# Kernel tuning notes

Hardware: AMD Instinct MI355X
Metric: run time of the kernel (lower is better)

The kernel has to match this reference:

```python
import jax, jax.numpy as jnp
import numpy as np

MAX_OBJECTS = 20
NODE_FEAT_DIM = 16
N_COLORS = 10
N_OPS = 8
HID = 64
RANK = 4
B = 32768


def _layer_norm(x, gamma, beta, eps=1e-5):
    mu = x.mean(-1, keepdims=True)
    var = ((x - mu) ** 2).mean(-1, keepdims=True)
    return (x - mu) / jnp.sqrt(var + eps) * gamma + beta


def setup_inputs() -> dict:
    key = jax.random.key(0)
    ks = jax.random.split(key, 32)
    lin = lambda k, i, o: jax.random.normal(k, (i, o), jnp.float32) * (1.0 / np.sqrt(i))
    d = {}
    d['nf'] = jax.random.normal(ks[0], (B, MAX_OBJECTS, NODE_FEAT_DIM), jnp.float32)
    d['nn_c'] = jax.random.randint(ks[1], (B,), 1, MAX_OBJECTS + 1)
    # ne + its LoRA adapter
    d['ne_W'] = lin(ks[2], NODE_FEAT_DIM, HID); d['ne_b'] = jnp.zeros((HID,), jnp.float32)
    d['ne_A'] = jax.random.normal(ks[3], (NODE_FEAT_DIM, RANK), jnp.float32) * 0.01
    d['ne_B'] = jax.random.normal(ks[4], (RANK, HID), jnp.float32) * 0.01
    # g1: Linear(2*hid,hid) [LoRA-wrapped] then Linear(hid,hid); relu applied after in lora path
    d['g1_W0'] = lin(ks[5], 2 * HID, HID); d['g1_b0'] = jnp.zeros((HID,), jnp.float32)
    d['g1_A'] = jax.random.normal(ks[6], (2 * HID, RANK), jnp.float32) * 0.01
    d['g1_B'] = jax.random.normal(ks[7], (RANK, HID), jnp.float32) * 0.01
    d['g1_W2'] = lin(ks[8], HID, HID); d['g1_b2'] = jnp.zeros((HID,), jnp.float32)
    d['g2_W0'] = lin(ks[9], 2 * HID, HID); d['g2_b0'] = jnp.zeros((HID,), jnp.float32)
    d['g2_A'] = jax.random.normal(ks[10], (2 * HID, RANK), jnp.float32) * 0.01
    d['g2_B'] = jax.random.normal(ks[11], (RANK, HID), jnp.float32) * 0.01
    d['g2_W2'] = lin(ks[12], HID, HID); d['g2_b2'] = jnp.zeros((HID,), jnp.float32)
    d['n1_g'] = jnp.ones((HID,), jnp.float32); d['n1_b'] = jnp.zeros((HID,), jnp.float32)
    d['n2_g'] = jnp.ones((HID,), jnp.float32); d['n2_b'] = jnp.zeros((HID,), jnp.float32)
    d['oh_W'] = lin(ks[13], HID, N_OPS); d['oh_b'] = jnp.zeros((N_OPS,), jnp.float32)
    d['c1_W'] = lin(ks[14], HID, N_COLORS); d['c1_b'] = jnp.zeros((N_COLORS,), jnp.float32)
    d['c2_W'] = lin(ks[15], HID, N_COLORS); d['c2_b'] = jnp.zeros((N_COLORS,), jnp.float32)
    d['pq_W'] = lin(ks[16], HID, HID); d['pq_b'] = jnp.zeros((HID,), jnp.float32)
    d['pk_W'] = lin(ks[17], HID, HID); d['pk_b'] = jnp.zeros((HID,), jnp.float32)
    return d


def reference(nf, nn_c, ne_W, ne_b, ne_A, ne_B,
              g1_W0, g1_b0, g1_A, g1_B, g1_W2, g1_b2,
              g2_W0, g2_b0, g2_A, g2_B, g2_W2, g2_b2,
              n1_g, n1_b, n2_g, n2_b,
              oh_W, oh_b, c1_W, c1_b, c2_W, c2_b, pq_W, pq_b, pk_W, pk_b):
    mask = jnp.arange(MAX_OBJECTS)[None, :] < nn_c[:, None]            # [B, N]
    mf = mask.astype(nf.dtype)[..., None]                              # [B, N, 1]
    denom = jnp.clip(mf.sum(1, keepdims=True), 1.0, None)              # [B, 1, 1]

    # node embedding with LoRA
    h = nf @ ne_W + ne_b + (nf @ ne_A) @ ne_B                          # [B, N, hid]

    def gnn_layer(h, W0, b0, A, Bm, W2, b2, lg, lb):
        msg = (h * mf).sum(1, keepdims=True) / denom                   # [B, 1, hid]
        cat = jnp.concatenate([h, jnp.broadcast_to(msg, h.shape)], -1) # [B, N, 2*hid]
        z = cat @ W0 + b0 + (cat @ A) @ Bm                             # LoRA linear
        h = h + jax.nn.relu(z @ W2 + b2)                               # relu AFTER second linear (lora path)
        return _layer_norm(h, lg, lb) * mf

    h = gnn_layer(h, g1_W0, g1_b0, g1_A, g1_B, g1_W2, g1_b2, n1_g, n1_b)
    h = gnn_layer(h, g2_W0, g2_b0, g2_A, g2_B, g2_W2, g2_b2, n2_g, n2_b)

    g = (h * mf).sum(1) / jnp.clip(mf.sum(1), 1.0, None)               # [B, hid]
    q = g @ pq_W + pq_b                                                # [B, hid]
    k = h @ pk_W + pk_b                                                # [B, N, hid]
    pl = jnp.einsum('bd,bnd->bn', q, k)
    pl = jnp.where(mask, pl, jnp.float32(-1e9))
    return (g @ oh_W + oh_b, g @ c1_W + c1_b, g @ c2_W + c2_b, pl, g)
```

## Files before the change

### kernel.cpp

```cpp
#include <hip/hip_runtime.h>

static constexpr int BATCH = 32768;

typedef short bf8 __attribute__((ext_vector_type(8)));
typedef float f32x4 __attribute__((ext_vector_type(4)));
typedef unsigned short u16x4 __attribute__((ext_vector_type(4)));

#define MFMA16 __builtin_amdgcn_mfma_f32_16x16x32_bf16


__device__ __forceinline__ unsigned short f2bf(float f) {
    return __builtin_bit_cast(unsigned short, static_cast<__bf16>(f));
}
__device__ __forceinline__ float bf2f(unsigned short h) {
    return __uint_as_float(((unsigned)h) << 16);
}

#define SWI(row, col)  ((row) * 64 + ((col) ^ (((row) & 7) << 3)))
#define LD8(buf, row, col8) (*(const bf8*)((buf) + (row) * 64 + 8 * ((col8) ^ ((row) & 7))))

__global__ void __launch_bounds__(256) merge_all(
    const float* __restrict__ neW, const float* __restrict__ neA, const float* __restrict__ neB,
    const float* __restrict__ ne_b,
    const float* __restrict__ g1W0, const float* __restrict__ g1A, const float* __restrict__ g1B,
    const float* __restrict__ g1W2, const float* __restrict__ g1b0, const float* __restrict__ g1b2,
    const float* __restrict__ g2W0, const float* __restrict__ g2A, const float* __restrict__ g2B,
    const float* __restrict__ g2W2, const float* __restrict__ g2b0, const float* __restrict__ g2b2,
    const float* __restrict__ pkW, const float* __restrict__ pqW,
    const float* __restrict__ ohW, const float* __restrict__ c1W, const float* __restrict__ c2W,
    const float* __restrict__ ohb, const float* __restrict__ c1b, const float* __restrict__ c2b,
    unsigned short* __restrict__ ws) {
    int t = blockIdx.x * 256 + threadIdx.x;
    if (t >= 28832) return;
    if (t >= 28768) {
        int n = t - 28768;
        float acc = g2b2[n];
        for (int k = 0; k < 64; ++k) acc = fmaf(g2b0[k], g2W2[k * 64 + n], acc);
        ((float*)ws)[14432 + n] = acc;
        return;
    }
    if (t >= 28704) {
        int n = t - 28704;
        float acc = g1b2[n];
        for (int k = 0; k < 64; ++k) acc = fmaf(g1b0[k], g1W2[k * 64 + n], acc);
        ((float*)ws)[14368 + n] = acc;
        return;
    }
    if (t >= 28672) {
        int i = t - 28672;
        float v = 0.0f;
        if (i < 8) v = ohb[i]; else if (i < 18) v = c1b[i - 8]; else if (i < 28) v = c2b[i - 18];
        ((float*)ws)[14336 + i] = v;
        return;
    }
    float val = 0.0f;
    if (t < 2048) {
        int n = t >> 5, k = t & 31;
        if (k < 16) {
            val = neW[k * 64 + n];
            #pragma unroll
            for (int r = 0; r < 4; ++r) val = fmaf(neA[k * 4 + r], neB[r * 64 + n], val);
        } else if (k == 16) {
            val = ne_b[n];
        }
    } else if (t < 18432) {
        int loc = t - 2048;
        const float *W0, *A, *Bm, *W2;
        if (loc < 8192) { W0 = g1W0; A = g1A; Bm = g1B; W2 = g1W2; }
        else { loc -= 8192; W0 = g2W0; A = g2A; Bm = g2B; W2 = g2W2; }
        int n = loc >> 7, k = loc & 127;
        float a0 = A[k * 4 + 0], a1 = A[k * 4 + 1], a2 = A[k * 4 + 2], a3 = A[k * 4 + 3];
        for (int j = 0; j < 64; ++j) {
            float w0e = W0[k * 64 + j];
            w0e = fmaf(a0, Bm[0 * 64 + j], w0e);
            w0e = fmaf(a1, Bm[1 * 64 + j], w0e);
            w0e = fmaf(a2, Bm[2 * 64 + j], w0e);
            w0e = fmaf(a3, Bm[3 * 64 + j], w0e);
            val = fmaf(w0e, W2[j * 64 + n], val);
        }
    } else if (t < 22528) {
        int loc = t - 18432; int n = loc >> 6, k = loc & 63;
        val = pkW[k * 64 + n];
    } else if (t < 26624) {
        int loc = t - 22528; int n = loc >> 6, k = loc & 63;
        val = pqW[k * 64 + n];
    } else {
        int loc = t - 26624; int n = loc >> 6, k = loc & 63;
        if (n < 8) val = ohW[k * 8 + n];
        else if (n < 18) val = c1W[k * 10 + (n - 8)];
        else if (n < 28) val = c2W[k * 10 + (n - 18)];
    }
    ws[t] = f2bf(val);
}

__device__ __forceinline__ int nc_sel(int4 nc, int bb) {
    int lo = (bb & 1) ? nc.y : nc.x;
    int hi = (bb & 1) ? nc.w : nc.z;
    return (bb & 2) ? hi : lo;
}

__device__ __forceinline__ void wave_mean(
    const unsigned short* hbuf, unsigned short* msgbuf, float* out4,
    int4 nc, int b0, int g, int c) {
    int c4 = c * 4;
    float s0 = 0, s1 = 0, s2 = 0, s3 = 0;
    int base = g * 20;
    #pragma unroll
    for (int n = 0; n < 20; ++n) {
        int row = base + n;
        u16x4 v = *(const u16x4*)(hbuf + SWI(row, c4));
        s0 += bf2f(v[0]); s1 += bf2f(v[1]); s2 += bf2f(v[2]); s3 += bf2f(v[3]);
    }
    float ic = 1.0f / (float)nc_sel(nc, g);
    s0 *= ic; s1 *= ic; s2 *= ic; s3 *= ic;
    u16x4 o; o[0] = f2bf(s0); o[1] = f2bf(s1); o[2] = f2bf(s2); o[3] = f2bf(s3);
    *(u16x4*)(msgbuf + SWI(g, c4)) = o;
    if (out4) {
        f32x4 fo = {s0, s1, s2, s3};
        *(f32x4*)(out4 + (size_t)(b0 + g) * 64 + c4) = fo;
    }
}

__device__ __forceinline__ void gnn_layer_sw(
    unsigned short* hbuf, unsigned short* msgbuf,
    const unsigned short* __restrict__ w02t,
    const float* __restrict__ b2e, const float* __restrict__ gmp, const float* __restrict__ btp,
    int4 nc, unsigned vmask, int b0, int g, int c) {
    wave_mean(hbuf, msgbuf, nullptr, nc, b0, g, c);
    const int nb = g * 4;

    #pragma unroll 1
    for (int mt = 0; mt < 5; ++mt) {
        int rA = mt * 16 + c;
        int bA = (rA >= 20) + (rA >= 40) + (rA >= 60);
        bf8 h0 = LD8(hbuf, rA, 0 + g);
        bf8 h1 = LD8(hbuf, rA, 4 + g);
        bf8 m0 = LD8(msgbuf, bA, 0 + g);
        bf8 m1 = LD8(msgbuf, bA, 4 + g);
        f32x4 du[4];
        #pragma unroll
        for (int nt = 0; nt < 4; ++nt) du[nt] = (f32x4){0.f, 0.f, 0.f, 0.f};
        #pragma unroll
        for (int nt = 0; nt < 4; ++nt) {
            const unsigned short* wp = w02t + (nt * 16 + c) * 128 + g * 8;
            du[nt] = MFMA16(*(const bf8*)(wp), h0, du[nt], 0, 0, 0);
            du[nt] = MFMA16(*(const bf8*)(wp + 32), h1, du[nt], 0, 0, 0);
            du[nt] = MFMA16(*(const bf8*)(wp + 64), m0, du[nt], 0, 0, 0);
            du[nt] = MFMA16(*(const bf8*)(wp + 96), m1, du[nt], 0, 0, 0);
        }
        float ps = 0.f, pq = 0.f;
        #pragma unroll
        for (int nt = 0; nt < 4; ++nt) {
            f32x4 b4 = *(const f32x4*)(b2e + nt * 16 + nb);
            u16x4 h4 = *(const u16x4*)(hbuf + SWI(rA, nt * 16 + nb));
            #pragma unroll
            for (int r = 0; r < 4; ++r) {
                float u = du[nt][r] + b4[r];
                float v = bf2f(h4[r]) + fmaxf(u, 0.f);
                du[nt][r] = v;
                ps += v; pq += v * v;
            }
        }
        ps += __shfl_xor(ps, 16, 64); ps += __shfl_xor(ps, 32, 64);
        pq += __shfl_xor(pq, 16, 64); pq += __shfl_xor(pq, 32, 64);
        float mu = ps * 0.015625f;
        float var = pq * 0.015625f - mu * mu;
        float rstd = rsqrtf(var + 1e-5f);
        bool valid = (vmask >> mt) & 1u;
        #pragma unroll
        for (int nt = 0; nt < 4; ++nt) {
            f32x4 g4 = *(const f32x4*)(gmp + nt * 16 + nb);
            f32x4 t4 = *(const f32x4*)(btp + nt * 16 + nb);
            u16x4 o;
            #pragma unroll
            for (int r = 0; r < 4; ++r) {
                float hn = (du[nt][r] - mu) * rstd * g4[r] + t4[r];
                o[r] = f2bf(valid ? hn : 0.f);
            }
            *(u16x4*)(hbuf + SWI(rA, nt * 16 + nb)) = o;
        }
    }
}

__global__ void __launch_bounds__(64, 5) gnn_main(
    const float* __restrict__ nf, const int* __restrict__ nn_c,
    const unsigned short* __restrict__ W,
    const float* __restrict__ n1g, const float* __restrict__ n1b,
    const float* __restrict__ n2g, const float* __restrict__ n2b,
    const float* __restrict__ pqb, const float* __restrict__ pkb,
    float* __restrict__ out) {
    __shared__ __align__(16) unsigned short hbuf[80 * 64];
    __shared__ __align__(16) unsigned short msgbuf[4 * 64];
    __shared__ __align__(16) float qbuf[4 * 68];

    const int lane = threadIdx.x & 63;
    const int g = lane >> 4, c = lane & 15;
    const int nb = g * 4;
    const int b0 = blockIdx.x * 4;
    const long grow0 = (long)b0 * 20;

    const unsigned short* neWt  = W;
    const unsigned short* w02t1 = W + 2048;
    const unsigned short* w02t2 = W + 10240;
    const unsigned short* pkt   = W + 18432;
    const unsigned short* pqt   = W + 22528;
    const unsigned short* hdt   = W + 26624;
    const float* wsf = (const float*)W;
    const float* headb = wsf + 14336;

    const size_t OUT1 = (size_t)BATCH * 8,  OUT2 = (size_t)BATCH * 18;
    const size_t OUT3 = (size_t)BATCH * 28, OUT4 = (size_t)BATCH * 48;

    int4 nc;
    nc.x = nn_c[b0 + 0]; nc.y = nn_c[b0 + 1];
    nc.z = nn_c[b0 + 2]; nc.w = nn_c[b0 + 3];

    unsigned vmask = 0;

    {
        bf8 bne[4];
        #pragma unroll
        for (int nt = 0; nt < 4; ++nt)
            bne[nt] = *(const bf8*)(neWt + (nt * 16 + c) * 32 + g * 8);
        f32x4 xc = (f32x4){0.f, 0.f, 0.f, 0.f}, yc = xc, xn = xc, yn = xc;
        if (g < 2) {
            const f32x4* p4 = (const f32x4*)(nf + (grow0 + c) * 16 + g * 8);
            xc = p4[0]; yc = p4[1];
        }
        #pragma unroll 1
        for (int mt = 0; mt < 5; ++mt) {
            int rA = mt * 16 + c;
            int bq = (rA >= 20) + (rA >= 40) + (rA >= 60);
            if (mt < 4 && g < 2) {
                const f32x4* p4 = (const f32x4*)(nf + (grow0 + rA + 16) * 16 + g * 8);
                xn = p4[0]; yn = p4[1];
            }
            bf8 b = (bf8){0, 0, 0, 0, 0, 0, 0, 0};
            if (g < 2) {
                b[0] = (short)f2bf(xc[0]); b[1] = (short)f2bf(xc[1]);
                b[2] = (short)f2bf(xc[2]); b[3] = (short)f2bf(xc[3]);
                b[4] = (short)f2bf(yc[0]); b[5] = (short)f2bf(yc[1]);
                b[6] = (short)f2bf(yc[2]); b[7] = (short)f2bf(yc[3]);
            } else if (g == 2) {
                b[0] = (short)0x3F80;
            }
            f32x4 acc[4];
            #pragma unroll
            for (int nt = 0; nt < 4; ++nt) acc[nt] = (f32x4){0.f, 0.f, 0.f, 0.f};
            #pragma unroll
            for (int nt = 0; nt < 4; ++nt) acc[nt] = MFMA16(bne[nt], b, acc[nt], 0, 0, 0);
            bool valid = (rA - bq * 20) < nc_sel(nc, bq);
            vmask |= (valid ? 1u : 0u) << mt;
            #pragma unroll
            for (int nt = 0; nt < 4; ++nt) {
                u16x4 o;
                #pragma unroll
                for (int r = 0; r < 4; ++r) o[r] = f2bf(valid ? acc[nt][r] : 0.f);
                *(u16x4*)(hbuf + SWI(rA, nt * 16 + nb)) = o;
            }
            xc = xn; yc = yn;
        }
    }

    gnn_layer_sw(hbuf, msgbuf, w02t1, wsf + 14368, n1g, n1b, nc, vmask, b0, g, c);
    gnn_layer_sw(hbuf, msgbuf, w02t2, wsf + 14432, n2g, n2b, nc, vmask, b0, g, c);

    wave_mean(hbuf, msgbuf, out + OUT4, nc, b0, g, c);

    {
        bf8 a0 = LD8(msgbuf, (c & 3), 0 + g);
        bf8 a1 = LD8(msgbuf, (c & 3), 4 + g);
        f32x4 dq[4];
        #pragma unroll
        for (int nt = 0; nt < 4; ++nt) dq[nt] = (f32x4){0.f, 0.f, 0.f, 0.f};
        #pragma unroll
        for (int nt = 0; nt < 4; ++nt) {
            const unsigned short* wp = pqt + (nt * 16 + c) * 64 + g * 8;
            dq[nt] = MFMA16(a0, *(const bf8*)(wp), dq[nt], 0, 0, 0);
            dq[nt] = MFMA16(a1, *(const bf8*)(wp + 32), dq[nt], 0, 0, 0);
        }
        f32x4 dh[2];
        #pragma unroll
        for (int nt = 0; nt < 2; ++nt) dh[nt] = (f32x4){0.f, 0.f, 0.f, 0.f};
        #pragma unroll
        for (int nt = 0; nt < 2; ++nt) {
            const unsigned short* wp = hdt + (nt * 16 + c) * 64 + g * 8;
            dh[nt] = MFMA16(a0, *(const bf8*)(wp), dh[nt], 0, 0, 0);
            dh[nt] = MFMA16(a1, *(const bf8*)(wp + 32), dh[nt], 0, 0, 0);
        }
        if (g == 0) {
            #pragma unroll
            for (int r = 0; r < 4; ++r) {
                #pragma unroll
                for (int nt = 0; nt < 4; ++nt)
                    qbuf[r * 68 + nt * 16 + c] = dq[nt][r] + pqb[nt * 16 + c];
                size_t ob = (size_t)(b0 + r);
                #pragma unroll
                for (int nt = 0; nt < 2; ++nt) {
                    int col = nt * 16 + c;
                    float v = dh[nt][r] + headb[col];
                    if (col < 8)       out[ob * 8 + col] = v;
                    else if (col < 18) out[OUT1 + ob * 10 + (col - 8)] = v;
                    else if (col < 28) out[OUT2 + ob * 10 + (col - 18)] = v;
                }
            }
        }
    }

    {
        #pragma unroll 1
        for (int mt = 0; mt < 5; ++mt) {
            int rA = mt * 16 + c;
            int bA = (rA >= 20) + (rA >= 40) + (rA >= 60);
            bf8 h0 = LD8(hbuf, rA, 0 + g);
            bf8 h1 = LD8(hbuf, rA, 4 + g);
            f32x4 dk[4];
            #pragma unroll
            for (int nt = 0; nt < 4; ++nt) dk[nt] = (f32x4){0.f, 0.f, 0.f, 0.f};
            #pragma unroll
            for (int nt = 0; nt < 4; ++nt) {
                const unsigned short* wp = pkt + (nt * 16 + c) * 64 + g * 8;
                dk[nt] = MFMA16(*(const bf8*)(wp), h0, dk[nt], 0, 0, 0);
                dk[nt] = MFMA16(*(const bf8*)(wp + 32), h1, dk[nt], 0, 0, 0);
            }
            float pl = 0.f;
            #pragma unroll
            for (int nt = 0; nt < 4; ++nt) {
                f32x4 q4 = *(const f32x4*)(&qbuf[bA * 68 + nt * 16 + nb]);
                f32x4 p4 = *(const f32x4*)(pkb + nt * 16 + nb);
                #pragma unroll
                for (int r = 0; r < 4; ++r)
                    pl = fmaf(dk[nt][r] + p4[r], q4[r], pl);
            }
            pl += __shfl_xor(pl, 16, 64);
            pl += __shfl_xor(pl, 32, 64);
            if (g == 0) {
                bool valid = (vmask >> mt) & 1u;
                out[OUT3 + (size_t)(grow0 + rA)] = valid ? pl : -1e9f;
            }
        }
    }
}

extern "C" void kernel_launch(void* const* d_in, const int* in_sizes, int n_in,
                              void* d_out, int out_size, void* d_ws, size_t ws_size,
                              hipStream_t stream) {
    const float* nf   = (const float*)d_in[0];
    const int*   nn_c = (const int*)d_in[1];
    const float* neW  = (const float*)d_in[2];
    const float* ne_b = (const float*)d_in[3];
    const float* neA  = (const float*)d_in[4];
    const float* neB  = (const float*)d_in[5];
    const float* g1W0 = (const float*)d_in[6];
    const float* g1b0 = (const float*)d_in[7];
    const float* g1A  = (const float*)d_in[8];
    const float* g1B  = (const float*)d_in[9];
    const float* g1W2 = (const float*)d_in[10];
    const float* g1b2 = (const float*)d_in[11];
    const float* g2W0 = (const float*)d_in[12];
    const float* g2b0 = (const float*)d_in[13];
    const float* g2A  = (const float*)d_in[14];
    const float* g2B  = (const float*)d_in[15];
    const float* g2W2 = (const float*)d_in[16];
    const float* g2b2 = (const float*)d_in[17];
    const float* n1g  = (const float*)d_in[18];
    const float* n1b  = (const float*)d_in[19];
    const float* n2g  = (const float*)d_in[20];
    const float* n2b  = (const float*)d_in[21];
    const float* ohW  = (const float*)d_in[22];
    const float* ohb  = (const float*)d_in[23];
    const float* c1W  = (const float*)d_in[24];
    const float* c1b  = (const float*)d_in[25];
    const float* c2W  = (const float*)d_in[26];
    const float* c2b  = (const float*)d_in[27];
    const float* pqW  = (const float*)d_in[28];
    const float* pqb  = (const float*)d_in[29];
    const float* pkW  = (const float*)d_in[30];
    const float* pkb  = (const float*)d_in[31];
    unsigned short* ws = (unsigned short*)d_ws;
    float* out = (float*)d_out;

    merge_all<<<113, 256, 0, stream>>>(neW, neA, neB, ne_b,
                                       g1W0, g1A, g1B, g1W2, g1b0, g1b2,
                                       g2W0, g2A, g2B, g2W2, g2b0, g2b2,
                                       pkW, pqW, ohW, c1W, c2W,
                                       ohb, c1b, c2b, ws);
    gnn_main<<<BATCH / 4, 64, 0, stream>>>(nf, nn_c, ws,
                                           n1g, n1b, n2g, n2b,
                                           pqb, pkb, out);
}
```

Baseline: 102.8 us.

## Process eight graphs per single-wave block instead of four

Each 64-thread block now handles 8 batch graphs (160 node rows) instead of 4. The node-count reciprocals move into shared memory, and the mean reduction is reworked so each lane covers 8 columns of one graph. The intent is to amortize per-block weight fetches and launch overhead over more rows and to fill the 16-row q/head MFMA tile better. In exchange, LDS per block doubles, occupancy drops, and the min-blocks launch bound hint is removed, which may reduce latency hiding.

```diff
diff --git a/kernel.cpp b/kernel.cpp
--- a/kernel.cpp
+++ b/kernel.cpp
@@ -93,46 +93,51 @@
     ws[t] = f2bf(val);
 }
 
-__device__ __forceinline__ int nc_sel(int4 nc, int bb) {
-    int lo = (bb & 1) ? nc.y : nc.x;
-    int hi = (bb & 1) ? nc.w : nc.z;
-    return (bb & 2) ? hi : lo;
-}
-
-__device__ __forceinline__ void wave_mean(
-    const unsigned short* hbuf, unsigned short* msgbuf, float* out4,
-    int4 nc, int b0, int g, int c) {
-    int c4 = c * 4;
-    float s0 = 0, s1 = 0, s2 = 0, s3 = 0;
-    int base = g * 20;
+__device__ __forceinline__ void wave_mean8(
+    const unsigned short* hbuf, unsigned short* msgbuf, const float* ncf, float* out4,
+    int b0) {
+    int lane = threadIdx.x & 63;
+    int lb = lane >> 3;
+    int c8 = (lane & 7) * 8;
+    float s0 = 0, s1 = 0, s2 = 0, s3 = 0, s4 = 0, s5 = 0, s6 = 0, s7 = 0;
+    int base = lb * 20;
     #pragma unroll
     for (int n = 0; n < 20; ++n) {
         int row = base + n;
-        u16x4 v = *(const u16x4*)(hbuf + SWI(row, c4));
-        s0 += bf2f(v[0]); s1 += bf2f(v[1]); s2 += bf2f(v[2]); s3 += bf2f(v[3]);
-    }
-    float ic = 1.0f / (float)nc_sel(nc, g);
+        u16x4 v0 = *(const u16x4*)(hbuf + SWI(row, c8));
+        u16x4 v1 = *(const u16x4*)(hbuf + SWI(row, c8 + 4));
+        s0 += bf2f(v0[0]); s1 += bf2f(v0[1]); s2 += bf2f(v0[2]); s3 += bf2f(v0[3]);
+        s4 += bf2f(v1[0]); s5 += bf2f(v1[1]); s6 += bf2f(v1[2]); s7 += bf2f(v1[3]);
+    }
+    float ic = ncf[lb];
     s0 *= ic; s1 *= ic; s2 *= ic; s3 *= ic;
-    u16x4 o; o[0] = f2bf(s0); o[1] = f2bf(s1); o[2] = f2bf(s2); o[3] = f2bf(s3);
-    *(u16x4*)(msgbuf + SWI(g, c4)) = o;
+    s4 *= ic; s5 *= ic; s6 *= ic; s7 *= ic;
+    u16x4 o0, o1;
+    o0[0] = f2bf(s0); o0[1] = f2bf(s1); o0[2] = f2bf(s2); o0[3] = f2bf(s3);
+    o1[0] = f2bf(s4); o1[1] = f2bf(s5); o1[2] = f2bf(s6); o1[3] = f2bf(s7);
+    *(u16x4*)(msgbuf + SWI(lb, c8)) = o0;
+    *(u16x4*)(msgbuf + SWI(lb, c8 + 4)) = o1;
     if (out4) {
-        f32x4 fo = {s0, s1, s2, s3};
-        *(f32x4*)(out4 + (size_t)(b0 + g) * 64 + c4) = fo;
+        f32x4 f0 = {s0, s1, s2, s3};
+        f32x4 f1 = {s4, s5, s6, s7};
+        float* p = out4 + (size_t)(b0 + lb) * 64 + c8;
+        *(f32x4*)(p) = f0;
+        *(f32x4*)(p + 4) = f1;
     }
 }
 
 __device__ __forceinline__ void gnn_layer_sw(
-    unsigned short* hbuf, unsigned short* msgbuf,
+    unsigned short* hbuf, unsigned short* msgbuf, const float* ncf,
     const unsigned short* __restrict__ w02t,
     const float* __restrict__ b2e, const float* __restrict__ gmp, const float* __restrict__ btp,
-    int4 nc, unsigned vmask, int b0, int g, int c) {
-    wave_mean(hbuf, msgbuf, nullptr, nc, b0, g, c);
+    unsigned vmask, int b0, int g, int c) {
+    wave_mean8(hbuf, msgbuf, ncf, nullptr, b0);
     const int nb = g * 4;
 
     #pragma unroll 1
-    for (int mt = 0; mt < 5; ++mt) {
+    for (int mt = 0; mt < 10; ++mt) {
         int rA = mt * 16 + c;
-        int bA = (rA >= 20) + (rA >= 40) + (rA >= 60);
+        int bA = rA / 20;
         bf8 h0 = LD8(hbuf, rA, 0 + g);
         bf8 h1 = LD8(hbuf, rA, 4 + g);
         bf8 m0 = LD8(msgbuf, bA, 0 + g);
@@ -182,21 +187,23 @@
     }
 }
 
-__global__ void __launch_bounds__(64, 5) gnn_main(
+__global__ void __launch_bounds__(64) gnn_main(
     const float* __restrict__ nf, const int* __restrict__ nn_c,
     const unsigned short* __restrict__ W,
     const float* __restrict__ n1g, const float* __restrict__ n1b,
     const float* __restrict__ n2g, const float* __restrict__ n2b,
     const float* __restrict__ pqb, const float* __restrict__ pkb,
     float* __restrict__ out) {
-    __shared__ __align__(16) unsigned short hbuf[80 * 64];
-    __shared__ __align__(16) unsigned short msgbuf[4 * 64];
-    __shared__ __align__(16) float qbuf[4 * 68];
+    __shared__ __align__(16) unsigned short hbuf[160 * 64];
+    __shared__ __align__(16) unsigned short msgbuf[8 * 64];
+    __shared__ __align__(16) float qbuf[8 * 68];
+    __shared__ int   nci[8];
+    __shared__ float ncf[8];
 
     const int lane = threadIdx.x & 63;
     const int g = lane >> 4, c = lane & 15;
     const int nb = g * 4;
-    const int b0 = blockIdx.x * 4;
+    const int b0 = blockIdx.x * 8;
     const long grow0 = (long)b0 * 20;
 
     const unsigned short* neWt  = W;
@@ -211,9 +218,11 @@
     const size_t OUT1 = (size_t)BATCH * 8,  OUT2 = (size_t)BATCH * 18;
     const size_t OUT3 = (size_t)BATCH * 28, OUT4 = (size_t)BATCH * 48;
 
-    int4 nc;
-    nc.x = nn_c[b0 + 0]; nc.y = nn_c[b0 + 1];
-    nc.z = nn_c[b0 + 2]; nc.w = nn_c[b0 + 3];
+    if (lane < 8) {
+        int v = nn_c[b0 + lane];
+        nci[lane] = v;
+        ncf[lane] = 1.0f / (float)v;
+    }
 
     unsigned vmask = 0;
 
@@ -228,10 +237,10 @@
             xc = p4[0]; yc = p4[1];
         }
         #pragma unroll 1
-        for (int mt = 0; mt < 5; ++mt) {
+        for (int mt = 0; mt < 10; ++mt) {
             int rA = mt * 16 + c;
-            int bq = (rA >= 20) + (rA >= 40) + (rA >= 60);
-            if (mt < 4 && g < 2) {
+            int bq = rA / 20;
+            if (mt < 9 && g < 2) {
                 const f32x4* p4 = (const f32x4*)(nf + (grow0 + rA + 16) * 16 + g * 8);
                 xn = p4[0]; yn = p4[1];
             }
@@ -249,7 +258,7 @@
             for (int nt = 0; nt < 4; ++nt) acc[nt] = (f32x4){0.f, 0.f, 0.f, 0.f};
             #pragma unroll
             for (int nt = 0; nt < 4; ++nt) acc[nt] = MFMA16(bne[nt], b, acc[nt], 0, 0, 0);
-            bool valid = (rA - bq * 20) < nc_sel(nc, bq);
+            bool valid = (rA - bq * 20) < nci[bq];
             vmask |= (valid ? 1u : 0u) << mt;
             #pragma unroll
             for (int nt = 0; nt < 4; ++nt) {
@@ -262,14 +271,14 @@
         }
     }
 
-    gnn_layer_sw(hbuf, msgbuf, w02t1, wsf + 14368, n1g, n1b, nc, vmask, b0, g, c);
-    gnn_layer_sw(hbuf, msgbuf, w02t2, wsf + 14432, n2g, n2b, nc, vmask, b0, g, c);
-
-    wave_mean(hbuf, msgbuf, out + OUT4, nc, b0, g, c);
+    gnn_layer_sw(hbuf, msgbuf, ncf, w02t1, wsf + 14368, n1g, n1b, vmask, b0, g, c);
+    gnn_layer_sw(hbuf, msgbuf, ncf, w02t2, wsf + 14432, n2g, n2b, vmask, b0, g, c);
+
+    wave_mean8(hbuf, msgbuf, ncf, out + OUT4, b0);
 
     {
-        bf8 a0 = LD8(msgbuf, (c & 3), 0 + g);
-        bf8 a1 = LD8(msgbuf, (c & 3), 4 + g);
+        bf8 a0 = LD8(msgbuf, (c & 7), 0 + g);
+        bf8 a1 = LD8(msgbuf, (c & 7), 4 + g);
         f32x4 dq[4];
         #pragma unroll
         for (int nt = 0; nt < 4; ++nt) dq[nt] = (f32x4){0.f, 0.f, 0.f, 0.f};
@@ -288,13 +297,14 @@
             dh[nt] = MFMA16(a0, *(const bf8*)(wp), dh[nt], 0, 0, 0);
             dh[nt] = MFMA16(a1, *(const bf8*)(wp + 32), dh[nt], 0, 0, 0);
         }
-        if (g == 0) {
+        if (g < 2) {
             #pragma unroll
             for (int r = 0; r < 4; ++r) {
+                int bb = g * 4 + r;
                 #pragma unroll
                 for (int nt = 0; nt < 4; ++nt)
-                    qbuf[r * 68 + nt * 16 + c] = dq[nt][r] + pqb[nt * 16 + c];
-                size_t ob = (size_t)(b0 + r);
+                    qbuf[bb * 68 + nt * 16 + c] = dq[nt][r] + pqb[nt * 16 + c];
+                size_t ob = (size_t)(b0 + bb);
                 #pragma unroll
                 for (int nt = 0; nt < 2; ++nt) {
                     int col = nt * 16 + c;
@@ -309,9 +319,9 @@
 
     {
         #pragma unroll 1
-        for (int mt = 0; mt < 5; ++mt) {
+        for (int mt = 0; mt < 10; ++mt) {
             int rA = mt * 16 + c;
-            int bA = (rA >= 20) + (rA >= 40) + (rA >= 60);
+            int bA = rA / 20;
             bf8 h0 = LD8(hbuf, rA, 0 + g);
             bf8 h1 = LD8(hbuf, rA, 4 + g);
             f32x4 dk[4];
@@ -385,7 +395,7 @@
                                        g2W0, g2A, g2B, g2W2, g2b0, g2b2,
                                        pkW, pqW, ohW, c1W, c2W,
                                        ohb, c1b, c2b, ws);
-    gnn_main<<<BATCH / 4, 64, 0, stream>>>(nf, nn_c, ws,
+    gnn_main<<<BATCH / 8, 64, 0, stream>>>(nf, nn_c, ws,
                                            n1g, n1b, n2g, n2b,
                                            pqb, pkb, out);
 }
```

Result: slower. 116.8 us (+13.6%).
